# Kernel tuning notes

Measured on AMD Instinct MI355X. Metric: run time of the kernel, lower is better.

## Reference

```python
import jax, jax.numpy as jnp
import numpy as np

DEPTH, B, S, E, H, EXP = 6, 16, 511, 1024, 16, 2
HD = E // H
FF = EXP * E


def _layernorm(x, g, b, eps=1e-5):
    m = jnp.mean(x, axis=-1, keepdims=True)
    v = jnp.var(x, axis=-1, keepdims=True)
    return (x - m) * jax.lax.rsqrt(v + eps) * g + b


def setup_inputs() -> dict:
    key = jax.random.key(0)
    ks = jax.random.split(key, 12)
    sc = 0.02
    inp = {
        "x": jax.random.normal(ks[0], (B, S, E), jnp.float32),
        "cls_token": jax.random.normal(ks[1], (1, 1, E), jnp.float32),
        "pos_emb": jax.random.normal(ks[2], (1, S + 1, E), jnp.float32),
        # attention projections (bias=False in source), stacked over depth
        "Wq": jax.random.normal(ks[3], (DEPTH, E, E), jnp.float32) * sc,
        "Wk": jax.random.normal(ks[4], (DEPTH, E, E), jnp.float32) * sc,
        "Wv": jax.random.normal(ks[5], (DEPTH, E, E), jnp.float32) * sc,
        "Wp": jax.random.normal(ks[6], (DEPTH, E, E), jnp.float32) * sc,
        # layernorm params
        "ln1_g": jnp.ones((DEPTH, E), jnp.float32),
        "ln1_b": jnp.zeros((DEPTH, E), jnp.float32),
        "ln2_g": jnp.ones((DEPTH, E), jnp.float32),
        "ln2_b": jnp.zeros((DEPTH, E), jnp.float32),
        # feed-forward (with bias, as nn.Linear default)
        "W1": jax.random.normal(ks[7], (DEPTH, E, FF), jnp.float32) * sc,
        "b1": jnp.zeros((DEPTH, FF), jnp.float32),
        "W2": jax.random.normal(ks[8], (DEPTH, FF, E), jnp.float32) * sc,
        "b2": jnp.zeros((DEPTH, E), jnp.float32),
    }
    return inp


def reference(x, cls_token, pos_emb, Wq, Wk, Wv, Wp,
              ln1_g, ln1_b, ln2_g, ln2_b, W1, b1, W2, b2):
    b = x.shape[0]
    # AddClsToken + PositionalEmbedding
    h = jnp.concatenate([jnp.broadcast_to(cls_token, (b, 1, E)), x], axis=1) + pos_emb
    scale = jnp.asarray(E ** 0.5, h.dtype)  # source scales by sqrt(emb_size)
    for i in range(DEPTH):
        # --- self-attention sublayer (pre-LN) ---
        res = h
        xn = _layernorm(h, ln1_g[i], ln1_b[i])
        q = (xn @ Wq[i]).reshape(b, -1, H, HD).transpose(0, 2, 1, 3)  # b h n d
        k = (xn @ Wk[i]).reshape(b, -1, H, HD).transpose(0, 2, 1, 3)
        v = (xn @ Wv[i]).reshape(b, -1, H, HD).transpose(0, 2, 1, 3)
        energy = jnp.einsum('bhqd,bhkd->bhqk', q, k)
        att = jax.nn.softmax(energy / scale, axis=-1)
        out = jnp.einsum('bhqk,bhkd->bhqd', att, v)
        out = out.transpose(0, 2, 1, 3).reshape(b, -1, E)
        h = out @ Wp[i] + res
        # --- feed-forward sublayer (pre-LN) ---
        res = h
        yn = _layernorm(h, ln2_g[i], ln2_b[i])
        ff = jax.nn.gelu(yn @ W1[i] + b1[i], approximate=False) @ W2[i] + b2[i]
        h = ff + res
    return h
```

## Files before the change

kernel.cpp:

```cpp
#include <hip/hip_runtime.h>
#include <cstdint>
#include <cstddef>

#define DEPTH 6
#define NB    16
#define NSEQ  512
#define EMB   1024
#define NHEAD 16
#define HDIM  64
#define FFD   2048
#define NTOK  (NB * NSEQ)

typedef unsigned short u16;
using bf16x8 = __attribute__((ext_vector_type(8))) __bf16;
using f32x4  = __attribute__((ext_vector_type(4))) float;
using u16x4  = __attribute__((ext_vector_type(4))) u16;
using u16x8  = __attribute__((ext_vector_type(8))) u16;

typedef __attribute__((address_space(1))) uint32_t* as1_u32p;
typedef __attribute__((address_space(3))) uint32_t* as3_u32p;
typedef __attribute__((address_space(3))) u16*      as3_u16p;

__device__ __forceinline__ u16 f2bf(float f) {
  union { float f; uint32_t u; } v; v.f = f;
  uint32_t u = v.u;
  return (u16)((u + 0x7FFFu + ((u >> 16) & 1u)) >> 16);
}

__device__ __forceinline__ void gload_lds16(const u16* g, u16* l) {
  void* gp = const_cast<u16*>(g);
  __builtin_amdgcn_global_load_lds((as1_u32p)gp, (as3_u32p)l, 16, 0, 0);
}

template<int ROWBYTES>
__device__ __forceinline__ void stage16k(const u16* g0, int ldk, u16* lds) {
  int t = threadIdx.x;
#pragma unroll
  for (int i = 0; i < 4; ++i) {
    int off = (i * 256 + t) * 16;
    int row = off / ROWBYTES;
    int pc  = (off % ROWBYTES) >> 4;
    int lc  = pc ^ (row & 7);
    gload_lds16(g0 + (size_t)row * ldk + lc * 8, lds + (off >> 1));
  }
}

__global__ __launch_bounds__(256)
void wprep_k(const float* __restrict__ W, u16* __restrict__ Wt,
             int K, int N, size_t inL, size_t outL, size_t outOff)
{
  int ntiles = N >> 6, ktiles = K >> 6;
  int bid = blockIdx.x;
  int l = bid / (ktiles * ntiles);
  int r = bid % (ktiles * ntiles);
  int kt = r / ntiles, nt = r % ntiles;
  const float* in = W + (size_t)l * inL + (size_t)(kt * 64) * N + nt * 64;
  u16* out = Wt + (size_t)l * outL + outOff + (size_t)(nt * 64) * K + kt * 64;
  __shared__ float tile[64][65];
  int t = threadIdx.x;
  int tr = t >> 4, tc = (t & 15) * 4;
#pragma unroll
  for (int i = 0; i < 4; ++i) {
    f32x4 v = *(const f32x4*)(in + (size_t)(tr + i * 16) * N + tc);
    tile[tr + i * 16][tc + 0] = v[0];
    tile[tr + i * 16][tc + 1] = v[1];
    tile[tr + i * 16][tc + 2] = v[2];
    tile[tr + i * 16][tc + 3] = v[3];
  }
  __syncthreads();
#pragma unroll
  for (int i = 0; i < 4; ++i) {
    int nr = tr + i * 16;
    u16x4 o;
    o[0] = f2bf(tile[tc + 0][nr]);
    o[1] = f2bf(tile[tc + 1][nr]);
    o[2] = f2bf(tile[tc + 2][nr]);
    o[3] = f2bf(tile[tc + 3][nr]);
    *(u16x4*)(out + (size_t)nr * K + tc) = o;
  }
}

__global__ __launch_bounds__(256)
void embed_k(const float* __restrict__ x, const float* __restrict__ cls,
             const float* __restrict__ pos, float* __restrict__ H)
{
  int row = blockIdx.x, t = threadIdx.x;
  int b_ = row >> 9, n = row & 511;
  int c = t * 4;
  f32x4 p = *(const f32x4*)(pos + (size_t)n * EMB + c);
  f32x4 s;
  if (n == 0) s = *(const f32x4*)(cls + c);
  else        s = *(const f32x4*)(x + ((size_t)b_ * 511 + (n - 1)) * EMB + c);
  f32x4 o = s + p;
  *(f32x4*)(H + (size_t)row * EMB + c) = o;
}

__global__ __launch_bounds__(256)
void ln_k(const float* __restrict__ H, const float* __restrict__ g,
          const float* __restrict__ b, u16* __restrict__ out)
{
  int row = blockIdx.x, t = threadIdx.x;
  const float* hp = H + (size_t)row * EMB;
  f32x4 v = *(const f32x4*)(hp + t * 4);
  float s  = v[0] + v[1] + v[2] + v[3];
  float ss = v[0]*v[0] + v[1]*v[1] + v[2]*v[2] + v[3]*v[3];
#pragma unroll
  for (int m = 1; m <= 32; m <<= 1) { s += __shfl_xor(s, m); ss += __shfl_xor(ss, m); }
  __shared__ float red[8];
  if ((t & 63) == 0) { red[(t >> 6) * 2] = s; red[(t >> 6) * 2 + 1] = ss; }
  __syncthreads();
  float S  = red[0] + red[2] + red[4] + red[6];
  float SS = red[1] + red[3] + red[5] + red[7];
  float mean = S * (1.0f / EMB);
  float var  = SS * (1.0f / EMB) - mean * mean;
  float rs = rsqrtf(var + 1e-5f);
  f32x4 gg = *(const f32x4*)(g + t * 4);
  f32x4 bb = *(const f32x4*)(b + t * 4);
  u16x4 o;
#pragma unroll
  for (int i = 0; i < 4; ++i) o[i] = f2bf((v[i] - mean) * rs * gg[i] + bb[i]);
  *(u16x4*)(out + (size_t)row * EMB + t * 4) = o;
}

template<int EPI>
__global__ __launch_bounds__(256, 3)
void gemm_k(const u16* __restrict__ A, const u16* __restrict__ Bt,
            int nbn, int K,
            const float* __restrict__ bias, float* __restrict__ H,
            u16* __restrict__ outB,
            u16* __restrict__ qo, u16* __restrict__ ko, u16* __restrict__ vto)
{
  __shared__ u16 sm[16384];
  int cpx = gridDim.x >> 3;
  int logical = (blockIdx.x & 7) * cpx + (blockIdx.x >> 3);
  int bm = logical / nbn, bn = logical % nbn;
  int t = threadIdx.x, lane = t & 63, w = t >> 6;
  int wm = w >> 1, wn = w & 1;
  const u16* Ab = A  + (size_t)(bm * 128) * K;
  const u16* Bb = Bt + (size_t)(bn * 128) * K;
  int nkt = K >> 6;

  const f32x4 vzero = {0.f, 0.f, 0.f, 0.f};
  f32x4 acc[4][4];
#pragma unroll
  for (int i = 0; i < 4; ++i)
#pragma unroll
    for (int j = 0; j < 4; ++j) acc[i][j] = vzero;

  int r0 = lane & 15;
  int hi = lane >> 4;
  int kk0 = hi * 8;

  for (int kt = 0; kt < nkt; ++kt) {
    stage16k<128>(Ab + kt * 64, K, sm);
    stage16k<128>(Bb + kt * 64, K, sm + 8192);
    __syncthreads();
    const char* smAp = (const char*)sm;
    const char* smBp = (const char*)(sm + 8192);
#pragma unroll
    for (int ks = 0; ks < 2; ++ks) {
      int kk = ks * 32 + kk0;
      bf16x8 a[4], b[4];
#pragma unroll
      for (int mf = 0; mf < 4; ++mf) {
        int row = wm * 64 + mf * 16 + r0;
        a[mf] = *(const bf16x8*)(smAp + row * 128 + ((kk * 2) ^ ((row & 7) << 4)));
      }
#pragma unroll
      for (int nf = 0; nf < 4; ++nf) {
        int row = wn * 64 + nf * 16 + r0;
        b[nf] = *(const bf16x8*)(smBp + row * 128 + ((kk * 2) ^ ((row & 7) << 4)));
      }
#pragma unroll
      for (int mf = 0; mf < 4; ++mf)
#pragma unroll
        for (int nf = 0; nf < 4; ++nf)
          acc[mf][nf] = __builtin_amdgcn_mfma_f32_16x16x32_bf16(a[mf], b[nf], acc[mf][nf], 0, 0, 0);
    }
    __syncthreads();
  }

  if (EPI == 1 || EPI == 3) {
    int m0 = bm * 128 + wm * 64;
    int n0 = bn * 128 + wn * 64;
#pragma unroll
    for (int mf = 0; mf < 4; ++mf) {
#pragma unroll
      for (int nf = 0; nf < 4; ++nf) {
        int col  = n0 + nf * 16 + r0;
        int rowb = m0 + mf * 16 + hi * 4;
#pragma unroll
        for (int j = 0; j < 4; ++j) {
          float v = acc[mf][nf][j];
          size_t idx = (size_t)(rowb + j) * EMB + col;
          if (EPI == 1) H[idx] = v + H[idx];
          else          H[idx] = v + bias[col] + H[idx];
        }
      }
    }
    return;
  }

  int sec = (bn * 128) >> 10;
  bool vsec = (EPI == 0) && (sec == 2);
#pragma unroll
  for (int mf = 0; mf < 4; ++mf) {
#pragma unroll
    for (int nf = 0; nf < 4; ++nf) {
      int colL = wn * 64 + nf * 16 + r0;
#pragma unroll
      for (int j = 0; j < 4; ++j) {
        int rowL = wm * 64 + mf * 16 + hi * 4 + j;
        float v = acc[mf][nf][j];
        if (EPI == 2) {
          float xg = v + bias[bn * 128 + colL];
          v = 0.5f * xg * (1.0f + erff(xg * 0.70710678118654752f));
        }
        u16 o = f2bf(v);
        if (!vsec)
          sm[rowL * 128 + (colL & 7) + ((((colL >> 3) ^ (rowL & 7))) << 3)] = o;
        else
          sm[colL * 128 + (rowL & 7) + ((((rowL >> 3) ^ (colL & 7))) << 3)] = o;
      }
    }
  }
  __syncthreads();

  int c  = t & 15;
  int rb = t >> 4;
  if (!vsec) {
#pragma unroll
    for (int i = 0; i < 8; ++i) {
      int row = rb * 8 + i;
      u16x8 v = *(const u16x8*)(sm + row * 128 + ((c ^ (row & 7)) << 3));
      if (EPI == 2) {
        int rowg = bm * 128 + row;
        int colg = bn * 128 + c * 8;
        *(u16x8*)(outB + (size_t)rowg * FFD + colg) = v;
      } else {
        int n_ = bm * 128 + row;
        int b_ = n_ >> 9, tok = n_ & 511;
        int c0 = (bn * 128 - sec * 1024) + c * 8;
        int hh = c0 >> 6, d0 = c0 & 63;
        u16* dst = (sec == 0) ? qo : ko;
        *(u16x8*)(dst + (((size_t)(b_ * NHEAD + hh) * NSEQ + tok) * HDIM) + d0) = v;
      }
    }
  } else {
#pragma unroll
    for (int i = 0; i < 8; ++i) {
      int rowp = rb * 8 + i;
      u16x8 v = *(const u16x8*)(sm + rowp * 128 + ((c ^ (rowp & 7)) << 3));
      int c0 = (bn * 128 - 2048) + rowp;
      int hh = c0 >> 6, d = c0 & 63;
      int tok0 = bm * 128 + c * 8;
      int b_ = tok0 >> 9;
      *(u16x8*)(vto + ((size_t)(b_ * NHEAD + hh) * HDIM + d) * NSEQ + (tok0 & 511)) = v;
    }
  }
}

__global__ __launch_bounds__(256, 3)
void attn_k(const u16* __restrict__ Q, const u16* __restrict__ Kk,
            const u16* __restrict__ Vt, u16* __restrict__ AO)
{
  __shared__ u16 kv[2][8192];
  __shared__ u16 Pt[4][2048];
  int bid = blockIdx.x;
  int bh = (bid & 7) * 32 + (bid >> 6);
  int qt = (bid >> 3) & 7;
  int t = threadIdx.x, lane = t & 63, w = t >> 6;
  const u16* Kb = Kk + (size_t)bh * (NSEQ * HDIM);
  const u16* Vb = Vt + (size_t)bh * (HDIM * NSEQ);
  int r0 = lane & 15, hi = lane >> 4, kk0 = hi * 8;

  int qrow = qt * 64 + w * 16 + r0;
  const u16* Qp = Q + ((size_t)bh * NSEQ + qrow) * HDIM;
  bf16x8 qf0 = *(const bf16x8*)(Qp + kk0);
  bf16x8 qf1 = *(const bf16x8*)(Qp + 32 + kk0);

  const f32x4 vzero = {0.f, 0.f, 0.f, 0.f};
  f32x4 accS[32];
#pragma unroll
  for (int f = 0; f < 32; ++f) accS[f] = vzero;

  stage16k<128>(Kb, HDIM, &kv[0][0]);
  __syncthreads();
#pragma unroll
  for (int kt = 0; kt < 4; ++kt) {
    if (kt < 3) stage16k<128>(Kb + (size_t)(kt + 1) * 128 * HDIM, HDIM, &kv[(kt + 1) & 1][0]);
    const char* smK = (const char*)&kv[kt & 1][0];
#pragma unroll
    for (int nfl = 0; nfl < 8; ++nfl) {
      int krow = nfl * 16 + r0;
      int swz = (krow & 7) << 4;
      bf16x8 b0 = *(const bf16x8*)(smK + krow * 128 + (((kk0)      * 2) ^ swz));
      bf16x8 b1 = *(const bf16x8*)(smK + krow * 128 + (((32 + kk0) * 2) ^ swz));
      accS[kt * 8 + nfl] = __builtin_amdgcn_mfma_f32_16x16x32_bf16(qf0, b0, accS[kt * 8 + nfl], 0, 0, 0);
      accS[kt * 8 + nfl] = __builtin_amdgcn_mfma_f32_16x16x32_bf16(qf1, b1, accS[kt * 8 + nfl], 0, 0, 0);
    }
    __syncthreads();
  }

  stage16k<256>(Vb, NSEQ, &kv[0][0]);

  float mx[4], den[4], rden[4];
#pragma unroll
  for (int j = 0; j < 4; ++j) {
    float m = -1e30f;
#pragma unroll
    for (int f = 0; f < 32; ++f) m = fmaxf(m, accS[f][j]);
    m = fmaxf(m, __shfl_xor(m, 1));
    m = fmaxf(m, __shfl_xor(m, 2));
    m = fmaxf(m, __shfl_xor(m, 4));
    m = fmaxf(m, __shfl_xor(m, 8));
    mx[j] = m;
    den[j] = 0.f;
  }
  uint32_t pb[64];
#pragma unroll
  for (int f = 0; f < 32; ++f) {
    float p0 = __expf((accS[f][0] - mx[0]) * 0.03125f);
    float p1 = __expf((accS[f][1] - mx[1]) * 0.03125f);
    float p2 = __expf((accS[f][2] - mx[2]) * 0.03125f);
    float p3 = __expf((accS[f][3] - mx[3]) * 0.03125f);
    den[0] += p0; den[1] += p1; den[2] += p2; den[3] += p3;
    pb[f * 2 + 0] = (uint32_t)f2bf(p0) | ((uint32_t)f2bf(p1) << 16);
    pb[f * 2 + 1] = (uint32_t)f2bf(p2) | ((uint32_t)f2bf(p3) << 16);
  }
#pragma unroll
  for (int j = 0; j < 4; ++j) {
    float d = den[j];
    d += __shfl_xor(d, 1); d += __shfl_xor(d, 2);
    d += __shfl_xor(d, 4); d += __shfl_xor(d, 8);
    rden[j] = 1.0f / d;
  }
  __syncthreads();

  int perm0 = ((r0 & 4) << 2) + ((r0 >> 3) << 2) + (r0 & 3);
  uint32_t ptb = (uint32_t)(uintptr_t)(as3_u16p)&Pt[w][0];
  uint32_t trBase = ptb + r0 * 2 + hi * 128;
  char* PtW = (char*)&Pt[w][0];

  f32x4 accO[4];
#pragma unroll
  for (int nf = 0; nf < 4; ++nf) accO[nf] = vzero;

#pragma unroll
  for (int kt = 0; kt < 4; ++kt) {
    if (kt < 3) stage16k<256>(Vb + (kt + 1) * 128, NSEQ, &kv[(kt + 1) & 1][0]);
#pragma unroll
    for (int fl = 0; fl < 8; ++fl) {
      int f = kt * 8 + fl;
      int row = (fl >> 1) * 32 + perm0 + ((fl & 1) << 3);
      *(uint2*)(PtW + row * 32 + hi * 8) = make_uint2(pb[f * 2], pb[f * 2 + 1]);
    }
    asm volatile("s_waitcnt lgkmcnt(0)" ::: "memory");
    const char* smV = (const char*)&kv[kt & 1][0];
#pragma unroll
    for (int s = 0; s < 4; ++s) {
      uint2 t0, t1;
      uint32_t a0 = trBase + s * 1024;
      asm volatile("ds_read_b64_tr_b16 %0, %1" : "=v"(t0) : "v"(a0) : "memory");
      asm volatile("ds_read_b64_tr_b16 %0, %1" : "=v"(t1) : "v"(a0 + 512) : "memory");
      bf16x8 vb[4];
#pragma unroll
      for (int nf = 0; nf < 4; ++nf) {
        int d = nf * 16 + r0;
        int inrow = s * 64 + hi * 16;
        vb[nf] = *(const bf16x8*)(smV + d * 256 + (inrow ^ ((d & 7) << 4)));
      }
      asm volatile("s_waitcnt lgkmcnt(0)" ::: "memory");
      __builtin_amdgcn_sched_barrier(0);
      union { uint4 u; bf16x8 v; } pa;
      pa.u = make_uint4(t0.x, t0.y, t1.x, t1.y);
#pragma unroll
      for (int nf = 0; nf < 4; ++nf)
        accO[nf] = __builtin_amdgcn_mfma_f32_16x16x32_bf16(pa.v, vb[nf], accO[nf], 0, 0, 0);
    }
    __syncthreads();
  }

  int b_ = bh >> 4, hh = bh & 15;
#pragma unroll
  for (int nf = 0; nf < 4; ++nf)
#pragma unroll
    for (int j = 0; j < 4; ++j) {
      int ql = hi * 4 + j;
      int tok = qt * 64 + w * 16 + ql;
      int col = hh * 64 + nf * 16 + r0;
      AO[((size_t)(b_ * NSEQ + tok)) * EMB + col] = f2bf(accO[nf][j] * rden[j]);
    }
}

extern "C" void kernel_launch(void* const* d_in, const int* in_sizes, int n_in,
                              void* d_out, int out_size, void* d_ws, size_t ws_size,
                              hipStream_t stream)
{
  const float* x    = (const float*)d_in[0];
  const float* cls  = (const float*)d_in[1];
  const float* pos  = (const float*)d_in[2];
  const float* Wq   = (const float*)d_in[3];
  const float* Wk   = (const float*)d_in[4];
  const float* Wv   = (const float*)d_in[5];
  const float* Wp   = (const float*)d_in[6];
  const float* ln1g = (const float*)d_in[7];
  const float* ln1b = (const float*)d_in[8];
  const float* ln2g = (const float*)d_in[9];
  const float* ln2b = (const float*)d_in[10];
  const float* W1   = (const float*)d_in[11];
  const float* b1   = (const float*)d_in[12];
  const float* W2   = (const float*)d_in[13];
  const float* b2   = (const float*)d_in[14];
  float* H = (float*)d_out;

  char* ws = (char*)d_ws;
  u16* wqkv = (u16*)(ws + 0);
  u16* wp   = (u16*)(ws + 37748736);
  u16* w1t  = (u16*)(ws + 50331648);
  u16* w2t  = (u16*)(ws + 75497472);
  u16* xn   = (u16*)(ws + 100663296);
  u16* qb   = (u16*)(ws + 117440512);
  u16* kb   = (u16*)(ws + 134217728);
  u16* vtb  = (u16*)(ws + 150994944);
  u16* ffb  = qb;

  wprep_k<<<1536, 256, 0, stream>>>(Wq, wqkv, 1024, 1024, 1048576, 3145728, 0);
  wprep_k<<<1536, 256, 0, stream>>>(Wk, wqkv, 1024, 1024, 1048576, 3145728, 1048576);
  wprep_k<<<1536, 256, 0, stream>>>(Wv, wqkv, 1024, 1024, 1048576, 3145728, 2097152);
  wprep_k<<<1536, 256, 0, stream>>>(Wp, wp,   1024, 1024, 1048576, 1048576, 0);
  wprep_k<<<3072, 256, 0, stream>>>(W1, w1t,  1024, 2048, 2097152, 2097152, 0);
  wprep_k<<<3072, 256, 0, stream>>>(W2, w2t,  2048, 1024, 2097152, 2097152, 0);

  embed_k<<<NTOK, 256, 0, stream>>>(x, cls, pos, H);

  for (int l = 0; l < DEPTH; ++l) {
    ln_k<<<NTOK, 256, 0, stream>>>(H, ln1g + l * EMB, ln1b + l * EMB, xn);
    gemm_k<0><<<64 * 24, 256, 0, stream>>>(xn, wqkv + (size_t)l * 3145728, 24, 1024,
                                           nullptr, nullptr, nullptr, qb, kb, vtb);
    attn_k<<<2048, 256, 0, stream>>>(qb, kb, vtb, xn);
    gemm_k<1><<<64 * 8, 256, 0, stream>>>(xn, wp + (size_t)l * 1048576, 8, 1024,
                                          nullptr, H, nullptr, nullptr, nullptr, nullptr);
    ln_k<<<NTOK, 256, 0, stream>>>(H, ln2g + l * EMB, ln2b + l * EMB, xn);
    gemm_k<2><<<64 * 16, 256, 0, stream>>>(xn, w1t + (size_t)l * 2097152, 16, 1024,
                                           b1 + l * FFD, nullptr, ffb, nullptr, nullptr, nullptr);
    gemm_k<3><<<64 * 8, 256, 0, stream>>>(ffb, w2t + (size_t)l * 2097152, 8, 2048,
                                          b2 + l * EMB, H, nullptr, nullptr, nullptr, nullptr);
  }
}
```

Measured before the change: 1.531 ms.

## Stage full K and V tiles into shared memory at once in attention

The attention kernel now loads the entire 512-row K block and the entire V block into a single 64KB shared buffer, replacing double-buffered 128-row chunks. This removes the per-chunk __syncthreads barriers in both the QK and PV loops. In exchange, shared memory use per block roughly doubles and launch bounds drop from 3 to 2 blocks per SM, which lowers occupancy and the latency hiding it gives.

```diff
diff --git a/kernel.cpp b/kernel.cpp
--- a/kernel.cpp
+++ b/kernel.cpp
@@ -260,11 +260,11 @@
   }
 }
 
-__global__ __launch_bounds__(256, 3)
+__global__ __launch_bounds__(256, 2)
 void attn_k(const u16* __restrict__ Q, const u16* __restrict__ Kk,
             const u16* __restrict__ Vt, u16* __restrict__ AO)
 {
-  __shared__ u16 kv[2][8192];
+  __shared__ u16 kvS[32768];
   __shared__ u16 Pt[4][2048];
   int bid = blockIdx.x;
   int bh = (bid & 7) * 32 + (bid >> 6);
@@ -284,25 +284,26 @@
 #pragma unroll
   for (int f = 0; f < 32; ++f) accS[f] = vzero;
 
-  stage16k<128>(Kb, HDIM, &kv[0][0]);
-  __syncthreads();
-#pragma unroll
-  for (int kt = 0; kt < 4; ++kt) {
-    if (kt < 3) stage16k<128>(Kb + (size_t)(kt + 1) * 128 * HDIM, HDIM, &kv[(kt + 1) & 1][0]);
-    const char* smK = (const char*)&kv[kt & 1][0];
-#pragma unroll
-    for (int nfl = 0; nfl < 8; ++nfl) {
-      int krow = nfl * 16 + r0;
-      int swz = (krow & 7) << 4;
-      bf16x8 b0 = *(const bf16x8*)(smK + krow * 128 + (((kk0)      * 2) ^ swz));
-      bf16x8 b1 = *(const bf16x8*)(smK + krow * 128 + (((32 + kk0) * 2) ^ swz));
-      accS[kt * 8 + nfl] = __builtin_amdgcn_mfma_f32_16x16x32_bf16(qf0, b0, accS[kt * 8 + nfl], 0, 0, 0);
-      accS[kt * 8 + nfl] = __builtin_amdgcn_mfma_f32_16x16x32_bf16(qf1, b1, accS[kt * 8 + nfl], 0, 0, 0);
-    }
-    __syncthreads();
-  }
-
-  stage16k<256>(Vb, NSEQ, &kv[0][0]);
+#pragma unroll
+  for (int i = 0; i < 4; ++i)
+    stage16k<128>(Kb + (size_t)i * 128 * HDIM, HDIM, kvS + i * 8192);
+  __syncthreads();
+
+  const char* smK = (const char*)kvS;
+#pragma unroll
+  for (int kf = 0; kf < 32; ++kf) {
+    int krow = kf * 16 + r0;
+    int swz = (krow & 7) << 4;
+    bf16x8 b0 = *(const bf16x8*)(smK + krow * 128 + (((kk0)      * 2) ^ swz));
+    bf16x8 b1 = *(const bf16x8*)(smK + krow * 128 + (((32 + kk0) * 2) ^ swz));
+    accS[kf] = __builtin_amdgcn_mfma_f32_16x16x32_bf16(qf0, b0, accS[kf], 0, 0, 0);
+    accS[kf] = __builtin_amdgcn_mfma_f32_16x16x32_bf16(qf1, b1, accS[kf], 0, 0, 0);
+  }
+  __syncthreads();
+
+#pragma unroll
+  for (int i = 0; i < 4; ++i)
+    stage16k<1024>(Vb + (size_t)i * 16 * NSEQ, NSEQ, kvS + i * 8192);
 
   float mx[4], den[4], rden[4];
 #pragma unroll
@@ -341,6 +342,7 @@
   uint32_t ptb = (uint32_t)(uintptr_t)(as3_u16p)&Pt[w][0];
   uint32_t trBase = ptb + r0 * 2 + hi * 128;
   char* PtW = (char*)&Pt[w][0];
+  const char* smV = (const char*)kvS;
 
   f32x4 accO[4];
 #pragma unroll
@@ -348,7 +350,6 @@
 
 #pragma unroll
   for (int kt = 0; kt < 4; ++kt) {
-    if (kt < 3) stage16k<256>(Vb + (kt + 1) * 128, NSEQ, &kv[(kt + 1) & 1][0]);
 #pragma unroll
     for (int fl = 0; fl < 8; ++fl) {
       int f = kt * 8 + fl;
@@ -356,7 +357,7 @@
       *(uint2*)(PtW + row * 32 + hi * 8) = make_uint2(pb[f * 2], pb[f * 2 + 1]);
     }
     asm volatile("s_waitcnt lgkmcnt(0)" ::: "memory");
-    const char* smV = (const char*)&kv[kt & 1][0];
+    __builtin_amdgcn_sched_barrier(0);
 #pragma unroll
     for (int s = 0; s < 4; ++s) {
       uint2 t0, t1;
@@ -364,11 +365,11 @@
       asm volatile("ds_read_b64_tr_b16 %0, %1" : "=v"(t0) : "v"(a0) : "memory");
       asm volatile("ds_read_b64_tr_b16 %0, %1" : "=v"(t1) : "v"(a0 + 512) : "memory");
       bf16x8 vb[4];
+      int kkv = kt * 128 + s * 32 + kk0;
 #pragma unroll
       for (int nf = 0; nf < 4; ++nf) {
         int d = nf * 16 + r0;
-        int inrow = s * 64 + hi * 16;
-        vb[nf] = *(const bf16x8*)(smV + d * 256 + (inrow ^ ((d & 7) << 4)));
+        vb[nf] = *(const bf16x8*)(smV + d * 1024 + ((kkv * 2) ^ ((d & 7) << 4)));
       }
       asm volatile("s_waitcnt lgkmcnt(0)" ::: "memory");
       __builtin_amdgcn_sched_barrier(0);
@@ -378,7 +379,6 @@
       for (int nf = 0; nf < 4; ++nf)
         accO[nf] = __builtin_amdgcn_mfma_f32_16x16x32_bf16(pa.v, vb[nf], accO[nf], 0, 0, 0);
     }
-    __syncthreads();
   }
 
   int b_ = bh >> 4, hh = bh & 15;
```

After: 1.525 ms. About the same (-0.4%).
